# Kernel optimization log

Hardware: AMD Instinct MI355X
Metric: run time of the kernel (lower is better)

The kernel has to match this reference:

```python
import jax, jax.numpy as jnp
import numpy as np
import math

B, T, D = 2, 2048, 1024
H, HD = 16, 64  # n_heads, head_dim; H*HD == D

def setup_inputs() -> dict:
    key = jax.random.key(0)
    ks = jax.random.split(key, 5)
    s = 1.0 / math.sqrt(D)
    return {
        "x": jax.random.normal(ks[0], (B, T, D), dtype=jnp.float32),
        "w_qkv": jax.random.normal(ks[1], (D, 3 * D), dtype=jnp.float32) * s,
        "b_qkv": jax.random.normal(ks[2], (3 * D,), dtype=jnp.float32) * 0.01,
        "w_o": jax.random.normal(ks[3], (D, D), dtype=jnp.float32) * s,
        "b_o": jax.random.normal(ks[4], (D,), dtype=jnp.float32) * 0.01,
    }

def reference(x, w_qkv, b_qkv, w_o, b_o):
    b, t, d_model = x.shape
    qkv = x @ w_qkv + b_qkv                       # [b,t,3d]
    q, k, v = jnp.split(qkv, 3, axis=-1)
    # [b,t,d] -> [b,h,t,hd]
    q = q.reshape(b, t, H, HD).transpose(0, 2, 1, 3)
    k = k.reshape(b, t, H, HD).transpose(0, 2, 1, 3)
    v = v.reshape(b, t, H, HD).transpose(0, 2, 1, 3)
    # NOTE: original scales by sqrt(d_model), not sqrt(head_dim)
    scores = jnp.einsum('bhqd,bhkd->bhqk', q, k) / math.sqrt(d_model)
    causal = jnp.tril(jnp.ones((t, t), dtype=bool))
    scores = jnp.where(causal[None, None], scores, -jnp.inf)
    # dropout p=0.0 (pre-softmax in original) is identity
    attn = jax.nn.softmax(scores, axis=-1)
    y = jnp.einsum('bhqk,bhkd->bhqd', attn, v)    # [b,h,t,hd]
    y = y.transpose(0, 2, 1, 3).reshape(b, t, d_model)
    return y @ w_o + b_o
```

## Files before the change

### kernel.cpp

```cpp
#include <hip/hip_runtime.h>
#include <math.h>

typedef __bf16 bf16;
typedef __bf16 bf16x4 __attribute__((ext_vector_type(4)));
typedef __bf16 bf16x8 __attribute__((ext_vector_type(8)));
typedef float f32x4 __attribute__((ext_vector_type(4)));

__device__ __forceinline__ void async_copy16(const void* g, void* l) {
  __builtin_amdgcn_global_load_lds(
      (__attribute__((address_space(1))) void*)(const_cast<void*>(g)),
      (__attribute__((address_space(3))) void*)(l),
      16, 0, 0);
}

__global__ __launch_bounds__(256) void convert_f32_bf16(
    const float* __restrict__ in, bf16* __restrict__ out) {
  int i = (blockIdx.x * 256 + threadIdx.x) * 4;
  float4 v = *(const float4*)(in + i);
  bf16x4 o;
  o[0] = (bf16)v.x; o[1] = (bf16)v.y; o[2] = (bf16)v.z; o[3] = (bf16)v.w;
  *(bf16x4*)(out + i) = o;
}

__global__ __launch_bounds__(256) void transpose_f32_bf16(
    const float* __restrict__ in, bf16* __restrict__ out, int R, int C) {
  __shared__ float tile[32][33];
  int bx = blockIdx.x * 32;
  int by = blockIdx.y * 32;
  int tx = threadIdx.x & 31;
  int ty = threadIdx.x >> 5;
#pragma unroll
  for (int i = 0; i < 32; i += 8)
    tile[ty + i][tx] = in[(size_t)(by + ty + i) * C + bx + tx];
  __syncthreads();
#pragma unroll
  for (int i = 0; i < 32; i += 8)
    out[(size_t)(bx + ty + i) * R + by + tx] = (bf16)tile[tx][ty + i];
}

__device__ __forceinline__ void gemm_mainloop(
    const bf16* __restrict__ A, const bf16* __restrict__ Bt, int K,
    int bm, int bn, bf16* As, bf16* Bs, f32x4 (&acc)[4][4]) {
  int tid = threadIdx.x;
  int w = tid >> 6, lane = tid & 63;
  int wm = w & 1, wn = w >> 1;
  int col = lane & 15, quad = lane >> 4;

  int srow = w * 32 + (lane >> 2);
  int scol = (lane & 3) * 8;
  const bf16* Ag0 = A + ((size_t)(bm * 128 + srow) * K + scol);
  const bf16* Bg0 = Bt + ((size_t)(bn * 128 + srow) * K + scol);
  bf16* AsW = As + (w * 32) * 32;
  bf16* BsW = Bs + (w * 32) * 32;

  for (int k0 = 0; k0 < K; k0 += 32) {
    __syncthreads();
    async_copy16(Ag0 + k0, AsW);
    async_copy16(Ag0 + k0 + (size_t)16 * K, AsW + 16 * 32);
    async_copy16(Bg0 + k0, BsW);
    async_copy16(Bg0 + k0 + (size_t)16 * K, BsW + 16 * 32);
    __syncthreads();

    bf16x8 af[4], bfr[4];
#pragma unroll
    for (int mi = 0; mi < 4; mi++)
      af[mi] = *(const bf16x8*)(As + (wm * 64 + mi * 16 + col) * 32 + quad * 8);
#pragma unroll
    for (int ni = 0; ni < 4; ni++)
      bfr[ni] = *(const bf16x8*)(Bs + (wn * 64 + ni * 16 + col) * 32 + quad * 8);
#pragma unroll
    for (int mi = 0; mi < 4; mi++)
#pragma unroll
      for (int ni = 0; ni < 4; ni++)
        acc[mi][ni] = __builtin_amdgcn_mfma_f32_16x16x32_bf16(
            af[mi], bfr[ni], acc[mi][ni], 0, 0, 0);
  }
}

__global__ __launch_bounds__(256) void gemm_qkv_kernel(
    const bf16* __restrict__ A, const bf16* __restrict__ Bt,
    const float* __restrict__ bias, bf16* __restrict__ qb,
    bf16* __restrict__ kb, bf16* __restrict__ vtb) {
  __shared__ bf16 As[128 * 32];
  __shared__ bf16 Bs[128 * 32];
  f32x4 acc[4][4] = {};
  int bm = blockIdx.x, bn = blockIdx.y;
  gemm_mainloop(A, Bt, 1024, bm, bn, As, Bs, acc);

  int tid = threadIdx.x;
  int w = tid >> 6, lane = tid & 63;
  int wm = w & 1, wn = w >> 1;
  int col = lane & 15, quad = lane >> 4;
#pragma unroll
  for (int ni = 0; ni < 4; ni++) {
    int gc = bn * 128 + wn * 64 + ni * 16 + col;
    float bv = bias[gc];
    int which = gc >> 10;
    int dd = gc & 1023;
    int h = dd >> 6, hd = dd & 63;
    if (which == 2) {
#pragma unroll
      for (int mi = 0; mi < 4; mi++) {
        int grow0 = bm * 128 + wm * 64 + mi * 16 + quad * 4;
        int b = grow0 >> 11, t0 = grow0 & 2047;
        bf16x4 pk;
#pragma unroll
        for (int r = 0; r < 4; r++) pk[r] = (bf16)(acc[mi][ni][r] + bv);
        *(bf16x4*)&vtb[(((size_t)(b * 16 + h) * 64 + hd) * 2048) + t0] = pk;
      }
    } else {
      bf16* dst = (which == 0) ? qb : kb;
#pragma unroll
      for (int mi = 0; mi < 4; mi++) {
#pragma unroll
        for (int r = 0; r < 4; r++) {
          int grow = bm * 128 + wm * 64 + mi * 16 + quad * 4 + r;
          int b = grow >> 11, t = grow & 2047;
          dst[(((size_t)(b * 16 + h) * 2048 + t) * 64) + hd] =
              (bf16)(acc[mi][ni][r] + bv);
        }
      }
    }
  }
}

__global__ __launch_bounds__(256) void gemm_out_kernel(
    const bf16* __restrict__ A, const bf16* __restrict__ Bt,
    const float* __restrict__ bias, float* __restrict__ outp) {
  __shared__ bf16 As[128 * 32];
  __shared__ bf16 Bs[128 * 32];
  f32x4 acc[4][4] = {};
  int bm = blockIdx.x, bn = blockIdx.y;
  gemm_mainloop(A, Bt, 1024, bm, bn, As, Bs, acc);

  int tid = threadIdx.x;
  int w = tid >> 6, lane = tid & 63;
  int wm = w & 1, wn = w >> 1;
  int col = lane & 15, quad = lane >> 4;
#pragma unroll
  for (int ni = 0; ni < 4; ni++) {
    int gc = bn * 128 + wn * 64 + ni * 16 + col;
    float bv = bias[gc];
#pragma unroll
    for (int mi = 0; mi < 4; mi++) {
#pragma unroll
      for (int r = 0; r < 4; r++) {
        int grow = bm * 128 + wm * 64 + mi * 16 + quad * 4 + r;
        outp[(size_t)grow * 1024 + gc] = acc[mi][ni][r] + bv;
      }
    }
  }
}

__global__ __launch_bounds__(256, 4) void attn_kernel(
    const bf16* __restrict__ qb, const bf16* __restrict__ kb,
    const bf16* __restrict__ vtb, bf16* __restrict__ y) {
  __shared__ bf16 Ks[64 * 64];
  __shared__ bf16 Vs[64 * 64];
  __shared__ bf16 Pl[4][16][72];

  int idx = blockIdx.x;
  int qt = 31 - (idx >> 5);
  int bh = idx & 31;
  int b = bh >> 4, h = bh & 15;
  int tid = threadIdx.x, w = tid >> 6, lane = tid & 63;
  int col = lane & 15, quad = lane >> 4;

  const bf16* Qh = qb + (size_t)bh * (2048 * 64);
  const bf16* Kh = kb + (size_t)bh * (2048 * 64);
  const bf16* Vth = vtb + (size_t)bh * (64 * 2048);

  int qrow = qt * 64 + w * 16 + col;
  bf16x8 aq[2];
#pragma unroll
  for (int ks = 0; ks < 2; ks++) {
    aq[ks] = *(const bf16x8*)(Qh + (size_t)qrow * 64 + ks * 32 + quad * 8);
#pragma unroll
    for (int e = 0; e < 8; e++)
      aq[ks][e] = (bf16)((float)aq[ks][e] * 0.03125f);
  }

  int r0 = w * 16 + (lane >> 3);
  int r1 = r0 + 8;
  int ch0 = (lane & 7) ^ (r0 & 7);
  int ch1 = (lane & 7) ^ (r1 & 7);
  size_t koff0 = (size_t)r0 * 64 + ch0 * 8;
  size_t koff1 = (size_t)r1 * 64 + ch1 * 8;
  size_t voff0 = (size_t)r0 * 2048 + ch0 * 8;
  size_t voff1 = (size_t)r1 * 2048 + ch1 * 8;
  bf16* KsW0 = Ks + (w * 16) * 64;
  bf16* KsW1 = Ks + (w * 16 + 8) * 64;
  bf16* VsW0 = Vs + (w * 16) * 64;
  bf16* VsW1 = Vs + (w * 16 + 8) * 64;

  float l_acc[4] = {0.f, 0.f, 0.f, 0.f};
  f32x4 o[4] = {};
  int qloc = w * 16 + quad * 4;

  for (int j = 0; j <= qt; j++) {
    __syncthreads();
    {
      const bf16* Kt = Kh + (size_t)j * 64 * 64;
      const bf16* Vt_ = Vth + (size_t)j * 64;
      async_copy16(Kt + koff0, KsW0);
      async_copy16(Kt + koff1, KsW1);
      async_copy16(Vt_ + voff0, VsW0);
      async_copy16(Vt_ + voff1, VsW1);
    }
    __syncthreads();

    f32x4 s[4] = {};
#pragma unroll
    for (int ks = 0; ks < 2; ks++)
#pragma unroll
      for (int c = 0; c < 4; c++) {
        int t = c * 16 + col;
        int slot = t * 8 + (((ks << 2) + quad) ^ (t & 7));
        bf16x8 bk = *(const bf16x8*)(Ks + slot * 8);
        s[c] = __builtin_amdgcn_mfma_f32_16x16x32_bf16(aq[ks], bk, s[c], 0, 0, 0);
      }

    bool diag = (j == qt);
#pragma unroll
    for (int c = 0; c < 4; c++) {
      int kloc = c * 16 + col;
#pragma unroll
      for (int r = 0; r < 4; r++) {
        float pv = (diag && kloc > qloc + r) ? 0.f : __expf(s[c][r]);
        l_acc[r] += pv;
        Pl[w][quad * 4 + r][c * 16 + col] = (bf16)pv;
      }
    }

    __builtin_amdgcn_sched_barrier(0);
    __builtin_amdgcn_s_waitcnt(0xc07f);
    __builtin_amdgcn_sched_barrier(0);

    bf16x8 ap0 = *(const bf16x8*)&Pl[w][col][quad * 8];
    bf16x8 ap1 = *(const bf16x8*)&Pl[w][col][32 + quad * 8];
#pragma unroll
    for (int ks = 0; ks < 2; ks++)
#pragma unroll
      for (int c = 0; c < 4; c++) {
        int d = c * 16 + col;
        int slot = d * 8 + (((ks << 2) + quad) ^ (d & 7));
        bf16x8 bv = *(const bf16x8*)(Vs + slot * 8);
        o[c] = __builtin_amdgcn_mfma_f32_16x16x32_bf16(
            ks == 0 ? ap0 : ap1, bv, o[c], 0, 0, 0);
      }
  }

#pragma unroll
  for (int r = 0; r < 4; r++) {
    float sum = l_acc[r];
    sum += __shfl_xor(sum, 1, 64);
    sum += __shfl_xor(sum, 2, 64);
    sum += __shfl_xor(sum, 4, 64);
    sum += __shfl_xor(sum, 8, 64);
    float inv = 1.f / sum;
    int t = qt * 64 + w * 16 + quad * 4 + r;
#pragma unroll
    for (int c = 0; c < 4; c++)
      y[((size_t)(b * 2048 + t)) * 1024 + h * 64 + c * 16 + col] =
          (bf16)(o[c][r] * inv);
  }
}

extern "C" void kernel_launch(void* const* d_in, const int* in_sizes, int n_in,
                              void* d_out, int out_size, void* d_ws,
                              size_t ws_size, hipStream_t stream) {
  const float* x = (const float*)d_in[0];
  const float* w_qkv = (const float*)d_in[1];
  const float* b_qkv = (const float*)d_in[2];
  const float* w_o = (const float*)d_in[3];
  const float* b_o = (const float*)d_in[4];
  float* out = (float*)d_out;

  char* p = (char*)d_ws;
  bf16* xb    = (bf16*)p; p += (size_t)4096 * 1024 * 2;
  bf16* wqkvT = (bf16*)p; p += (size_t)3072 * 1024 * 2;
  bf16* woT   = (bf16*)p; p += (size_t)1024 * 1024 * 2;
  bf16* qb    = (bf16*)p; p += (size_t)2 * 16 * 2048 * 64 * 2;
  bf16* kb    = (bf16*)p; p += (size_t)2 * 16 * 2048 * 64 * 2;
  bf16* vtb   = (bf16*)p; p += (size_t)2 * 16 * 64 * 2048 * 2;
  bf16* yb    = (bf16*)p; p += (size_t)4096 * 1024 * 2;

  convert_f32_bf16<<<4096 * 1024 / 1024, 256, 0, stream>>>(x, xb);
  transpose_f32_bf16<<<dim3(3072 / 32, 1024 / 32), 256, 0, stream>>>(
      w_qkv, wqkvT, 1024, 3072);
  transpose_f32_bf16<<<dim3(1024 / 32, 1024 / 32), 256, 0, stream>>>(
      w_o, woT, 1024, 1024);
  gemm_qkv_kernel<<<dim3(32, 24), 256, 0, stream>>>(
      xb, wqkvT, b_qkv, qb, kb, vtb);
  attn_kernel<<<1024, 256, 0, stream>>>(qb, kb, vtb, yb);
  gemm_out_kernel<<<dim3(32, 8), 256, 0, stream>>>(yb, woT, b_o, out);
}
```

Baseline: 178.9 us.

## Enlarge attention query tile to 128 rows per block for K/V reuse

Each attention block now handles 128 query rows instead of 64, with every wave computing two 16-row MFMA sub-tiles that share each loaded K/V tile. This halves the K/V global loads and LDS staging per query row and halves the grid to 512 blocks. In exchange it doubles accumulator registers, which may lower occupancy, and it adds an extra masked diagonal tile per block. With fewer, heavier blocks the causal load imbalance across CUs may also get worse.

```diff
diff --git a/kernel.cpp b/kernel.cpp
--- a/kernel.cpp
+++ b/kernel.cpp
@@ -157,10 +157,10 @@
     const bf16* __restrict__ vtb, bf16* __restrict__ y) {
   __shared__ bf16 Ks[64 * 64];
   __shared__ bf16 Vs[64 * 64];
-  __shared__ bf16 Pl[4][16][72];
+  __shared__ bf16 Pl[4][32][72];
 
   int idx = blockIdx.x;
-  int qt = 31 - (idx >> 5);
+  int qt = 15 - (idx >> 5);
   int bh = idx & 31;
   int b = bh >> 4, h = bh & 15;
   int tid = threadIdx.x, w = tid >> 6, lane = tid & 63;
@@ -170,14 +170,18 @@
   const bf16* Kh = kb + (size_t)bh * (2048 * 64);
   const bf16* Vth = vtb + (size_t)bh * (64 * 2048);
 
-  int qrow = qt * 64 + w * 16 + col;
-  bf16x8 aq[2];
-#pragma unroll
-  for (int ks = 0; ks < 2; ks++) {
-    aq[ks] = *(const bf16x8*)(Qh + (size_t)qrow * 64 + ks * 32 + quad * 8);
-#pragma unroll
-    for (int e = 0; e < 8; e++)
-      aq[ks][e] = (bf16)((float)aq[ks][e] * 0.03125f);
+  bf16x8 aq[2][2];
+#pragma unroll
+  for (int mi = 0; mi < 2; mi++) {
+    int qrow = qt * 128 + w * 32 + mi * 16 + col;
+#pragma unroll
+    for (int ks = 0; ks < 2; ks++) {
+      aq[mi][ks] =
+          *(const bf16x8*)(Qh + (size_t)qrow * 64 + ks * 32 + quad * 8);
+#pragma unroll
+      for (int e = 0; e < 8; e++)
+        aq[mi][ks][e] = (bf16)((float)aq[mi][ks][e] * 0.03125f);
+    }
   }
 
   int r0 = w * 16 + (lane >> 3);
@@ -193,11 +197,11 @@
   bf16* VsW0 = Vs + (w * 16) * 64;
   bf16* VsW1 = Vs + (w * 16 + 8) * 64;
 
-  float l_acc[4] = {0.f, 0.f, 0.f, 0.f};
-  f32x4 o[4] = {};
-  int qloc = w * 16 + quad * 4;
-
-  for (int j = 0; j <= qt; j++) {
+  float l_acc[2][4] = {};
+  f32x4 o[2][4] = {};
+
+  int jmax = 2 * qt + 1;
+  for (int j = 0; j <= jmax; j++) {
     __syncthreads();
     {
       const bf16* Kt = Kh + (size_t)j * 64 * 64;
@@ -209,7 +213,7 @@
     }
     __syncthreads();
 
-    f32x4 s[4] = {};
+    f32x4 s[2][4] = {};
 #pragma unroll
     for (int ks = 0; ks < 2; ks++)
 #pragma unroll
@@ -217,18 +221,25 @@
         int t = c * 16 + col;
         int slot = t * 8 + (((ks << 2) + quad) ^ (t & 7));
         bf16x8 bk = *(const bf16x8*)(Ks + slot * 8);
-        s[c] = __builtin_amdgcn_mfma_f32_16x16x32_bf16(aq[ks], bk, s[c], 0, 0, 0);
-      }
-
-    bool diag = (j == qt);
-#pragma unroll
-    for (int c = 0; c < 4; c++) {
-      int kloc = c * 16 + col;
-#pragma unroll
-      for (int r = 0; r < 4; r++) {
-        float pv = (diag && kloc > qloc + r) ? 0.f : __expf(s[c][r]);
-        l_acc[r] += pv;
-        Pl[w][quad * 4 + r][c * 16 + col] = (bf16)pv;
+#pragma unroll
+        for (int mi = 0; mi < 2; mi++)
+          s[mi][c] = __builtin_amdgcn_mfma_f32_16x16x32_bf16(aq[mi][ks], bk,
+                                                             s[mi][c], 0, 0, 0);
+      }
+
+    bool dtile = (j >= 2 * qt);
+#pragma unroll
+    for (int mi = 0; mi < 2; mi++) {
+      int qglob0 = qt * 128 + w * 32 + mi * 16 + quad * 4;
+#pragma unroll
+      for (int c = 0; c < 4; c++) {
+        int kglob = j * 64 + c * 16 + col;
+#pragma unroll
+        for (int r = 0; r < 4; r++) {
+          float pv = (dtile && kglob > qglob0 + r) ? 0.f : __expf(s[mi][c][r]);
+          l_acc[mi][r] += pv;
+          Pl[w][mi * 16 + quad * 4 + r][c * 16 + col] = (bf16)pv;
+        }
       }
     }
 
@@ -236,8 +247,12 @@
     __builtin_amdgcn_s_waitcnt(0xc07f);
     __builtin_amdgcn_sched_barrier(0);
 
-    bf16x8 ap0 = *(const bf16x8*)&Pl[w][col][quad * 8];
-    bf16x8 ap1 = *(const bf16x8*)&Pl[w][col][32 + quad * 8];
+    bf16x8 ap[2][2];
+#pragma unroll
+    for (int mi = 0; mi < 2; mi++) {
+      ap[mi][0] = *(const bf16x8*)&Pl[w][mi * 16 + col][quad * 8];
+      ap[mi][1] = *(const bf16x8*)&Pl[w][mi * 16 + col][32 + quad * 8];
+    }
 #pragma unroll
     for (int ks = 0; ks < 2; ks++)
 #pragma unroll
@@ -245,25 +260,29 @@
         int d = c * 16 + col;
         int slot = d * 8 + (((ks << 2) + quad) ^ (d & 7));
         bf16x8 bv = *(const bf16x8*)(Vs + slot * 8);
-        o[c] = __builtin_amdgcn_mfma_f32_16x16x32_bf16(
-            ks == 0 ? ap0 : ap1, bv, o[c], 0, 0, 0);
-      }
-  }
-
-#pragma unroll
-  for (int r = 0; r < 4; r++) {
-    float sum = l_acc[r];
-    sum += __shfl_xor(sum, 1, 64);
-    sum += __shfl_xor(sum, 2, 64);
-    sum += __shfl_xor(sum, 4, 64);
-    sum += __shfl_xor(sum, 8, 64);
-    float inv = 1.f / sum;
-    int t = qt * 64 + w * 16 + quad * 4 + r;
-#pragma unroll
-    for (int c = 0; c < 4; c++)
-      y[((size_t)(b * 2048 + t)) * 1024 + h * 64 + c * 16 + col] =
-          (bf16)(o[c][r] * inv);
-  }
+#pragma unroll
+        for (int mi = 0; mi < 2; mi++)
+          o[mi][c] = __builtin_amdgcn_mfma_f32_16x16x32_bf16(ap[mi][ks], bv,
+                                                             o[mi][c], 0, 0, 0);
+      }
+  }
+
+#pragma unroll
+  for (int mi = 0; mi < 2; mi++)
+#pragma unroll
+    for (int r = 0; r < 4; r++) {
+      float sum = l_acc[mi][r];
+      sum += __shfl_xor(sum, 1, 64);
+      sum += __shfl_xor(sum, 2, 64);
+      sum += __shfl_xor(sum, 4, 64);
+      sum += __shfl_xor(sum, 8, 64);
+      float inv = 1.f / sum;
+      int t = qt * 128 + w * 32 + mi * 16 + quad * 4 + r;
+#pragma unroll
+      for (int c = 0; c < 4; c++)
+        y[((size_t)(b * 2048 + t)) * 1024 + h * 64 + c * 16 + col] =
+            (bf16)(o[mi][c][r] * inv);
+    }
 }
 
 extern "C" void kernel_launch(void* const* d_in, const int* in_sizes, int n_in,
@@ -292,6 +311,6 @@
       w_o, woT, 1024, 1024);
   gemm_qkv_kernel<<<dim3(32, 24), 256, 0, stream>>>(
       xb, wqkvT, b_qkv, qb, kb, vtb);
-  attn_kernel<<<1024, 256, 0, stream>>>(qb, kb, vtb, yb);
+  attn_kernel<<<512, 256, 0, stream>>>(qb, kb, vtb, yb);
   gemm_out_kernel<<<dim3(32, 8), 256, 0, stream>>>(yb, woT, b_o, out);
 }
```

Measured after the change: 198.8 us. +11.1%, slower.

## Merge prep kernels into one launch and transpose attention MFMA operands

Applied to the files above, without the earlier changes.

The three preprocessing launches (x conversion and two weight transposes) are folded into a single prep_kernel that dispatches by block index, which removes two kernel launches and their gaps. The attention kernel swaps the MFMA operand order so it computes S^T and O^T. Each lane then holds four consecutive key or dim values for a single query, so P is written to LDS and y is written to global memory as packed bf16x4 stores instead of scalar stores. The row-sum reduction shrinks from four shuffles per row to two. The transposed layout changes which indices the causal mask compares, which must still be correct, and the P stores into LDS may now hit different bank-conflict patterns.

```diff
diff --git a/kernel.cpp b/kernel.cpp
--- a/kernel.cpp
+++ b/kernel.cpp
@@ -13,20 +13,11 @@
       16, 0, 0);
 }
 
-__global__ __launch_bounds__(256) void convert_f32_bf16(
-    const float* __restrict__ in, bf16* __restrict__ out) {
-  int i = (blockIdx.x * 256 + threadIdx.x) * 4;
-  float4 v = *(const float4*)(in + i);
-  bf16x4 o;
-  o[0] = (bf16)v.x; o[1] = (bf16)v.y; o[2] = (bf16)v.z; o[3] = (bf16)v.w;
-  *(bf16x4*)(out + i) = o;
-}
-
-__global__ __launch_bounds__(256) void transpose_f32_bf16(
-    const float* __restrict__ in, bf16* __restrict__ out, int R, int C) {
+__device__ __forceinline__ void transpose_tile(
+    const float* __restrict__ in, bf16* __restrict__ out, int R, int C,
+    int bxi, int byi) {
   __shared__ float tile[32][33];
-  int bx = blockIdx.x * 32;
-  int by = blockIdx.y * 32;
+  int bx = bxi * 32, by = byi * 32;
   int tx = threadIdx.x & 31;
   int ty = threadIdx.x >> 5;
 #pragma unroll
@@ -36,6 +27,26 @@
 #pragma unroll
   for (int i = 0; i < 32; i += 8)
     out[(size_t)(bx + ty + i) * R + by + tx] = (bf16)tile[tx][ty + i];
+}
+
+__global__ __launch_bounds__(256) void prep_kernel(
+    const float* __restrict__ x, bf16* __restrict__ xb,
+    const float* __restrict__ w_qkv, bf16* __restrict__ wqkvT,
+    const float* __restrict__ w_o, bf16* __restrict__ woT) {
+  int blk = blockIdx.x;
+  if (blk < 4096) {
+    int i = blk * 1024 + threadIdx.x * 4;
+    float4 v = *(const float4*)(x + i);
+    bf16x4 o;
+    o[0] = (bf16)v.x; o[1] = (bf16)v.y; o[2] = (bf16)v.z; o[3] = (bf16)v.w;
+    *(bf16x4*)(xb + i) = o;
+  } else if (blk < 7168) {
+    int tb = blk - 4096;
+    transpose_tile(w_qkv, wqkvT, 1024, 3072, tb % 96, tb / 96);
+  } else {
+    int tb = blk - 7168;
+    transpose_tile(w_o, woT, 1024, 1024, tb % 32, tb / 32);
+  }
 }
 
 __device__ __forceinline__ void gemm_mainloop(
@@ -193,9 +204,8 @@
   bf16* VsW0 = Vs + (w * 16) * 64;
   bf16* VsW1 = Vs + (w * 16 + 8) * 64;
 
-  float l_acc[4] = {0.f, 0.f, 0.f, 0.f};
-  f32x4 o[4] = {};
-  int qloc = w * 16 + quad * 4;
+  float l_part = 0.f;
+  f32x4 ot[4] = {};
 
   for (int j = 0; j <= qt; j++) {
     __syncthreads();
@@ -209,27 +219,31 @@
     }
     __syncthreads();
 
-    f32x4 s[4] = {};
+    f32x4 st[4] = {};
 #pragma unroll
     for (int ks = 0; ks < 2; ks++)
 #pragma unroll
       for (int c = 0; c < 4; c++) {
         int t = c * 16 + col;
         int slot = t * 8 + (((ks << 2) + quad) ^ (t & 7));
-        bf16x8 bk = *(const bf16x8*)(Ks + slot * 8);
-        s[c] = __builtin_amdgcn_mfma_f32_16x16x32_bf16(aq[ks], bk, s[c], 0, 0, 0);
+        bf16x8 ak = *(const bf16x8*)(Ks + slot * 8);
+        st[c] = __builtin_amdgcn_mfma_f32_16x16x32_bf16(ak, aq[ks], st[c],
+                                                        0, 0, 0);
       }
 
     bool diag = (j == qt);
+    int qglob = qt * 64 + w * 16 + col;
 #pragma unroll
     for (int c = 0; c < 4; c++) {
-      int kloc = c * 16 + col;
+      bf16x4 pk;
 #pragma unroll
       for (int r = 0; r < 4; r++) {
-        float pv = (diag && kloc > qloc + r) ? 0.f : __expf(s[c][r]);
-        l_acc[r] += pv;
-        Pl[w][quad * 4 + r][c * 16 + col] = (bf16)pv;
-      }
+        int tglob = j * 64 + c * 16 + quad * 4 + r;
+        float pv = (diag && tglob > qglob) ? 0.f : __expf(st[c][r]);
+        l_part += pv;
+        pk[r] = (bf16)pv;
+      }
+      *(bf16x4*)&Pl[w][col][c * 16 + quad * 4] = pk;
     }
 
     __builtin_amdgcn_sched_barrier(0);
@@ -244,25 +258,24 @@
       for (int c = 0; c < 4; c++) {
         int d = c * 16 + col;
         int slot = d * 8 + (((ks << 2) + quad) ^ (d & 7));
-        bf16x8 bv = *(const bf16x8*)(Vs + slot * 8);
-        o[c] = __builtin_amdgcn_mfma_f32_16x16x32_bf16(
-            ks == 0 ? ap0 : ap1, bv, o[c], 0, 0, 0);
-      }
-  }
-
-#pragma unroll
-  for (int r = 0; r < 4; r++) {
-    float sum = l_acc[r];
-    sum += __shfl_xor(sum, 1, 64);
-    sum += __shfl_xor(sum, 2, 64);
-    sum += __shfl_xor(sum, 4, 64);
-    sum += __shfl_xor(sum, 8, 64);
-    float inv = 1.f / sum;
-    int t = qt * 64 + w * 16 + quad * 4 + r;
-#pragma unroll
-    for (int c = 0; c < 4; c++)
-      y[((size_t)(b * 2048 + t)) * 1024 + h * 64 + c * 16 + col] =
-          (bf16)(o[c][r] * inv);
+        bf16x8 av = *(const bf16x8*)(Vs + slot * 8);
+        ot[c] = __builtin_amdgcn_mfma_f32_16x16x32_bf16(
+            av, ks == 0 ? ap0 : ap1, ot[c], 0, 0, 0);
+      }
+  }
+
+  float sum = l_part;
+  sum += __shfl_xor(sum, 16, 64);
+  sum += __shfl_xor(sum, 32, 64);
+  float inv = 1.f / sum;
+  int tq = qt * 64 + w * 16 + col;
+  bf16* yrow = y + ((size_t)(b * 2048 + tq)) * 1024 + h * 64;
+#pragma unroll
+  for (int c = 0; c < 4; c++) {
+    bf16x4 pk;
+#pragma unroll
+    for (int r = 0; r < 4; r++) pk[r] = (bf16)(ot[c][r] * inv);
+    *(bf16x4*)(yrow + c * 16 + quad * 4) = pk;
   }
 }
 
@@ -285,11 +298,7 @@
   bf16* vtb   = (bf16*)p; p += (size_t)2 * 16 * 64 * 2048 * 2;
   bf16* yb    = (bf16*)p; p += (size_t)4096 * 1024 * 2;
 
-  convert_f32_bf16<<<4096 * 1024 / 1024, 256, 0, stream>>>(x, xb);
-  transpose_f32_bf16<<<dim3(3072 / 32, 1024 / 32), 256, 0, stream>>>(
-      w_qkv, wqkvT, 1024, 3072);
-  transpose_f32_bf16<<<dim3(1024 / 32, 1024 / 32), 256, 0, stream>>>(
-      w_o, woT, 1024, 1024);
+  prep_kernel<<<8192, 256, 0, stream>>>(x, xb, w_qkv, wqkvT, w_o, woT);
   gemm_qkv_kernel<<<dim3(32, 24), 256, 0, stream>>>(
       xb, wqkvT, b_qkv, qb, kb, vtb);
   attn_kernel<<<1024, 256, 0, stream>>>(qb, kb, vtb, yb);
```

Result: no change. 179.3 us (+0.2%).
